# Kernel optimization log

Hardware: AMD Instinct MI355X
Metric: run time of the kernel (lower is better)

Reference implementation:

```python
import jax, jax.numpy as jnp
import numpy as np

WIN = 3
KER = 2 * WIN + 1
EPS = 1e-6


def _box_filter(x):
    """Separable 3D uniform box filter, mathematically identical to
    conv3d with a (1,1,k,k,k) kernel of ones/k^3 and padding=win.
    x: (B, 1, D, H, W) -> same shape."""
    dn = jax.lax.conv_dimension_numbers(x.shape, (1, 1, KER, 1, 1),
                                        ('NCDHW', 'OIDHW', 'NCDHW'))
    k1 = jnp.full((1, 1, KER, 1, 1), 1.0 / KER, dtype=x.dtype)
    k2 = jnp.full((1, 1, 1, KER, 1), 1.0 / KER, dtype=x.dtype)
    k3 = jnp.full((1, 1, 1, 1, KER), 1.0 / KER, dtype=x.dtype)
    x = jax.lax.conv_general_dilated(x, k1, (1, 1, 1),
                                     [(WIN, WIN), (0, 0), (0, 0)], dimension_numbers=dn)
    x = jax.lax.conv_general_dilated(x, k2, (1, 1, 1),
                                     [(0, 0), (WIN, WIN), (0, 0)], dimension_numbers=dn)
    x = jax.lax.conv_general_dilated(x, k3, (1, 1, 1),
                                     [(0, 0), (0, 0), (WIN, WIN)], dimension_numbers=dn)
    return x


def setup_inputs() -> dict:
    key = jax.random.key(0)
    kI, kJ = jax.random.split(key)
    shape = (2, 1, 160, 160, 160)
    I = jax.random.uniform(kI, shape, dtype=jnp.float32)
    J = jax.random.uniform(kJ, shape, dtype=jnp.float32)
    return {"I": I, "J": J}


def reference(I, J):
    I_mean = _box_filter(I)
    J_mean = _box_filter(J)
    I2_mean = _box_filter(I * I)
    J2_mean = _box_filter(J * J)
    IJ_mean = _box_filter(I * J)
    cross = IJ_mean - I_mean * J_mean
    I_var = I2_mean - I_mean * I_mean
    J_var = J2_mean - J_mean * J_mean
    lncc = cross * cross / (I_var * J_var + EPS)
    return -jnp.mean(lncc)
```

## Files before the change

### kernel.cpp

```cpp
#include <hip/hip_runtime.h>

#define DIM 160
#define TW 32
#define TH 16
#define RROWS (TH + 6)
#define CHUNK 16
#define NCHUNK (DIM / CHUNK)
#define NBATCH 2
#define NTOT 8192000.0f

__global__ __launch_bounds__(256) void lncc_fused_kernel(
    const float* __restrict__ I,
    const float* __restrict__ J,
    float* __restrict__ out)
{
    __shared__ __align__(16) float rs[2][5][RROWS][TW];
    __shared__ float wsum[4];

    const int tid = threadIdx.x;
    const int tx = tid & 15;
    const int ty = tid >> 4;
    const int rr = tid >> 3;
    const int rg = tid & 7;
    const bool rowActive = (rr < RROWS);

    const int tw0 = blockIdx.x * TW;
    const int th0 = blockIdx.y * TH;
    const int bz  = blockIdx.z;
    const int b     = bz / NCHUNK;
    const int chunk = bz - b * NCHUNK;
    const int z0  = chunk * CHUNK;

    const size_t plane = (size_t)DIM * DIM;
    const float* Ib = I + (size_t)b * DIM * plane;
    const float* Jb = J + (size_t)b * DIM * plane;

    const int gh = th0 + rr - 3;
    const bool rowValid = rowActive && ((unsigned)gh < (unsigned)DIM);
    const int gw0 = tw0 + 4 * rg - 4;
    const bool ok0 = (unsigned)gw0       <= (unsigned)(DIM - 4);
    const bool ok1 = (unsigned)(gw0 + 4) <= (unsigned)(DIM - 4);
    const bool ok2 = (unsigned)(gw0 + 8) <= (unsigned)(DIM - 4);
    const size_t rowbase = (size_t)gh * DIM + gw0;

    float rng[5][2][7];
#pragma unroll
    for (int f = 0; f < 5; ++f)
#pragma unroll
        for (int j = 0; j < 2; ++j)
#pragma unroll
            for (int k = 0; k < 7; ++k) rng[f][j][k] = 0.f;

    float S[5][2];
#pragma unroll
    for (int f = 0; f < 5; ++f) { S[f][0] = 0.f; S[f][1] = 0.f; }

    float acc = 0.f;
    int p = 0;

    for (int zin = z0 - 3; zin < z0 + CHUNK + 3; ++zin) {
        const bool zv = (zin >= 0) && (zin < DIM);
        float Cx[5], Cy[5];
#pragma unroll
        for (int f = 0; f < 5; ++f) { Cx[f] = 0.f; Cy[f] = 0.f; }

        if (zv) {
            if (rowActive) {
                float4 a0 = {0,0,0,0}, a1 = {0,0,0,0}, a2 = {0,0,0,0};
                float4 b0 = {0,0,0,0}, b1 = {0,0,0,0}, b2 = {0,0,0,0};
                if (rowValid) {
                    const float* Ip = Ib + (size_t)zin * plane + rowbase;
                    const float* Jp = Jb + (size_t)zin * plane + rowbase;
                    if (ok0) { a0 = *(const float4*)(Ip);     b0 = *(const float4*)(Jp);     }
                    if (ok1) { a1 = *(const float4*)(Ip + 4); b1 = *(const float4*)(Jp + 4); }
                    if (ok2) { a2 = *(const float4*)(Ip + 8); b2 = *(const float4*)(Jp + 8); }
                }
                float vI[12] = {a0.x,a0.y,a0.z,a0.w, a1.x,a1.y,a1.z,a1.w, a2.x,a2.y,a2.z,a2.w};
                float vJ[12] = {b0.x,b0.y,b0.z,b0.w, b1.x,b1.y,b1.z,b1.w, b2.x,b2.y,b2.z,b2.w};

                float sI=0.f, sJ=0.f, sI2=0.f, sJ2=0.f, sIJ=0.f;
#pragma unroll
                for (int i = 1; i < 8; ++i) {
                    float a = vI[i], c = vJ[i];
                    sI += a; sJ += c;
                    sI2 = fmaf(a, a, sI2);
                    sJ2 = fmaf(c, c, sJ2);
                    sIJ = fmaf(a, c, sIJ);
                }
                float wI[4], wJ[4], wI2[4], wJ2[4], wIJ[4];
                wI[0]=sI; wJ[0]=sJ; wI2[0]=sI2; wJ2[0]=sJ2; wIJ[0]=sIJ;
#pragma unroll
                for (int k = 1; k < 4; ++k) {
                    float an = vI[7+k], cn = vJ[7+k];
                    float ao = vI[k],   co = vJ[k];
                    sI  += an - ao;
                    sJ  += cn - co;
                    sI2 += fmaf(an, an, -(ao*ao));
                    sJ2 += fmaf(cn, cn, -(co*co));
                    sIJ += fmaf(an, cn, -(ao*co));
                    wI[k]=sI; wJ[k]=sJ; wI2[k]=sI2; wJ2[k]=sJ2; wIJ[k]=sIJ;
                }
                const int cc = 4 * rg;
                *(float4*)&rs[p][0][rr][cc] = make_float4(wI[0],  wI[1],  wI[2],  wI[3]);
                *(float4*)&rs[p][1][rr][cc] = make_float4(wJ[0],  wJ[1],  wJ[2],  wJ[3]);
                *(float4*)&rs[p][2][rr][cc] = make_float4(wI2[0], wI2[1], wI2[2], wI2[3]);
                *(float4*)&rs[p][3][rr][cc] = make_float4(wJ2[0], wJ2[1], wJ2[2], wJ2[3]);
                *(float4*)&rs[p][4][rr][cc] = make_float4(wIJ[0], wIJ[1], wIJ[2], wIJ[3]);
            }
            __syncthreads();

#pragma unroll
            for (int dr = 0; dr < 7; ++dr) {
                const int r = ty + dr;
#pragma unroll
                for (int f = 0; f < 5; ++f) {
                    const float2 v = *(const float2*)&rs[p][f][r][2 * tx];
                    Cx[f] += v.x;
                    Cy[f] += v.y;
                }
            }
            p ^= 1;
        }

#pragma unroll
        for (int f = 0; f < 5; ++f) {
            S[f][0] += Cx[f] - rng[f][0][0];
            S[f][1] += Cy[f] - rng[f][1][0];
#pragma unroll
            for (int k = 0; k < 6; ++k) {
                rng[f][0][k] = rng[f][0][k+1];
                rng[f][1][k] = rng[f][1][k+1];
            }
            rng[f][0][6] = Cx[f];
            rng[f][1][6] = Cy[f];
        }

        if (zin - 3 >= z0) {
            const float inv = 1.0f / 343.0f;
#pragma unroll
            for (int j = 0; j < 2; ++j) {
                float mI  = S[0][j] * inv;
                float mJ  = S[1][j] * inv;
                float mI2 = S[2][j] * inv;
                float mJ2 = S[3][j] * inv;
                float mIJ = S[4][j] * inv;
                float cross = mIJ - mI * mJ;
                float vI_ = mI2 - mI * mI;
                float vJ_ = mJ2 - mJ * mJ;
                acc += cross * cross / (vI_ * vJ_ + 1e-6f);
            }
        }
    }

#pragma unroll
    for (int off = 32; off > 0; off >>= 1)
        acc += __shfl_down(acc, off, 64);
    if ((tid & 63) == 0) wsum[tid >> 6] = acc;
    __syncthreads();
    if (tid == 0) {
        float t = wsum[0] + wsum[1] + wsum[2] + wsum[3];
        atomicAdd(out, t * (-1.0f / NTOT));
    }
}

extern "C" void kernel_launch(void* const* d_in, const int* in_sizes, int n_in,
                              void* d_out, int out_size, void* d_ws, size_t ws_size,
                              hipStream_t stream) {
    const float* I = (const float*)d_in[0];
    const float* J = (const float*)d_in[1];
    float* out = (float*)d_out;

    hipMemsetAsync(out, 0, sizeof(float), stream);

    dim3 grid(DIM / TW, DIM / TH, NBATCH * NCHUNK);
    dim3 block(256);
    lncc_fused_kernel<<<grid, block, 0, stream>>>(I, J, out);
}
```

Baseline: 153.5 us.

## Shrink z-chunks, unroll the ring buffer, and rescale the LNCC term to avoid division

Reduces the z-chunk from 16 to 10 slices, giving 16 chunks per batch and more blocks to spread across the CUs. The cost is more redundant halo slices per block: 16 loaded slices per 10 outputs instead of 22 per 16. The z ring buffer is now indexed by a compile-time slot in a 7-way unrolled step macro, replacing the per-step register shifting. The LNCC term works on raw sums scaled by 343, with a rescaled epsilon and a hardware reciprocal instead of a division. That adds a small approximation error from the fast reciprocal.

```diff
diff --git a/kernel.cpp b/kernel.cpp
--- a/kernel.cpp
+++ b/kernel.cpp
@@ -4,10 +4,65 @@
 #define TW 32
 #define TH 16
 #define RROWS (TH + 6)
-#define CHUNK 16
+#define CHUNK 10
 #define NCHUNK (DIM / CHUNK)
 #define NBATCH 2
 #define NTOT 8192000.0f
+#define EPS_S 13841.287f
+
+__device__ __forceinline__ void row_stage(
+    const float* __restrict__ Ip, const float* __restrict__ Jp,
+    bool rowValid, bool ok0, bool ok1, bool ok2,
+    float (* __restrict__ rsp)[RROWS][TW], int rr, int cc)
+{
+    float4 a0={0,0,0,0}, a1={0,0,0,0}, a2={0,0,0,0};
+    float4 b0={0,0,0,0}, b1={0,0,0,0}, b2={0,0,0,0};
+    if (rowValid) {
+        if (ok0) { a0 = *(const float4*)(Ip);     b0 = *(const float4*)(Jp);     }
+        if (ok1) { a1 = *(const float4*)(Ip + 4); b1 = *(const float4*)(Jp + 4); }
+        if (ok2) { a2 = *(const float4*)(Ip + 8); b2 = *(const float4*)(Jp + 8); }
+    }
+    float vI[12] = {a0.x,a0.y,a0.z,a0.w, a1.x,a1.y,a1.z,a1.w, a2.x,a2.y,a2.z,a2.w};
+    float vJ[12] = {b0.x,b0.y,b0.z,b0.w, b1.x,b1.y,b1.z,b1.w, b2.x,b2.y,b2.z,b2.w};
+
+    float sI=0.f, sJ=0.f, sI2=0.f, sJ2=0.f, sIJ=0.f;
+#pragma unroll
+    for (int i = 1; i < 8; ++i) {
+        float a = vI[i], c = vJ[i];
+        sI += a; sJ += c;
+        sI2 = fmaf(a, a, sI2);
+        sJ2 = fmaf(c, c, sJ2);
+        sIJ = fmaf(a, c, sIJ);
+    }
+    float wI[4], wJ[4], wI2[4], wJ2[4], wIJ[4];
+    wI[0]=sI; wJ[0]=sJ; wI2[0]=sI2; wJ2[0]=sJ2; wIJ[0]=sIJ;
+#pragma unroll
+    for (int k = 1; k < 4; ++k) {
+        float an = vI[7+k], cn = vJ[7+k];
+        float ao = vI[k],   co = vJ[k];
+        sI  += an - ao;
+        sJ  += cn - co;
+        sI2 += fmaf(an, an, -(ao*ao));
+        sJ2 += fmaf(cn, cn, -(co*co));
+        sIJ += fmaf(an, cn, -(ao*co));
+        wI[k]=sI; wJ[k]=sJ; wI2[k]=sI2; wJ2[k]=sJ2; wIJ[k]=sIJ;
+    }
+    *(float4*)&rsp[0][rr][cc] = make_float4(wI[0],  wI[1],  wI[2],  wI[3]);
+    *(float4*)&rsp[1][rr][cc] = make_float4(wJ[0],  wJ[1],  wJ[2],  wJ[3]);
+    *(float4*)&rsp[2][rr][cc] = make_float4(wI2[0], wI2[1], wI2[2], wI2[3]);
+    *(float4*)&rsp[3][rr][cc] = make_float4(wJ2[0], wJ2[1], wJ2[2], wJ2[3]);
+    *(float4*)&rsp[4][rr][cc] = make_float4(wIJ[0], wIJ[1], wIJ[2], wIJ[3]);
+}
+
+__device__ __forceinline__ float lncc_term(float SI, float SJ, float SI2,
+                                           float SJ2, float SIJ)
+{
+    float cross = fmaf(SIJ, 343.f, -(SI * SJ));
+    float vI    = fmaf(SI2, 343.f, -(SI * SI));
+    float vJ    = fmaf(SJ2, 343.f, -(SJ * SJ));
+    float den   = fmaf(vI, vJ, EPS_S);
+    return cross * cross * __builtin_amdgcn_rcpf(den);
+}
 
 __global__ __launch_bounds__(256) void lncc_fused_kernel(
     const float* __restrict__ I,
@@ -22,13 +77,14 @@
     const int ty = tid >> 4;
     const int rr = tid >> 3;
     const int rg = tid & 7;
+    const int cc = 4 * rg;
     const bool rowActive = (rr < RROWS);
 
     const int tw0 = blockIdx.x * TW;
     const int th0 = blockIdx.y * TH;
     const int bz  = blockIdx.z;
-    const int b     = bz / NCHUNK;
-    const int chunk = bz - b * NCHUNK;
+    const int b     = bz >> 4;
+    const int chunk = bz & 15;
     const int z0  = chunk * CHUNK;
 
     const size_t plane = (size_t)DIM * DIM;
@@ -37,120 +93,67 @@
 
     const int gh = th0 + rr - 3;
     const bool rowValid = rowActive && ((unsigned)gh < (unsigned)DIM);
-    const int gw0 = tw0 + 4 * rg - 4;
+    const int gw0 = tw0 + cc - 4;
     const bool ok0 = (unsigned)gw0       <= (unsigned)(DIM - 4);
     const bool ok1 = (unsigned)(gw0 + 4) <= (unsigned)(DIM - 4);
     const bool ok2 = (unsigned)(gw0 + 8) <= (unsigned)(DIM - 4);
-    const size_t rowbase = (size_t)gh * DIM + gw0;
+    const ptrdiff_t rowbase = (ptrdiff_t)gh * DIM + gw0;
+    const float* IpBase = Ib + rowbase;
+    const float* JpBase = Jb + rowbase;
 
-    float rng[5][2][7];
+    float rngx[5][7], rngy[5][7];
+    float Sx[5], Sy[5];
 #pragma unroll
-    for (int f = 0; f < 5; ++f)
+    for (int f = 0; f < 5; ++f) {
+        Sx[f] = 0.f; Sy[f] = 0.f;
 #pragma unroll
-        for (int j = 0; j < 2; ++j)
-#pragma unroll
-            for (int k = 0; k < 7; ++k) rng[f][j][k] = 0.f;
-
-    float S[5][2];
-#pragma unroll
-    for (int f = 0; f < 5; ++f) { S[f][0] = 0.f; S[f][1] = 0.f; }
+        for (int k = 0; k < 7; ++k) { rngx[f][k] = 0.f; rngy[f][k] = 0.f; }
+    }
 
     float acc = 0.f;
     int p = 0;
+    int zin = z0 - 3;
+    int s = 0;
 
-    for (int zin = z0 - 3; zin < z0 + CHUNK + 3; ++zin) {
-        const bool zv = (zin >= 0) && (zin < DIM);
-        float Cx[5], Cy[5];
-#pragma unroll
-        for (int f = 0; f < 5; ++f) { Cx[f] = 0.f; Cy[f] = 0.f; }
+#define STEP(SLOT) {                                                          \
+    const bool zv = ((unsigned)zin < (unsigned)DIM);                          \
+    float Cx[5] = {0.f,0.f,0.f,0.f,0.f};                                      \
+    float Cy[5] = {0.f,0.f,0.f,0.f,0.f};                                      \
+    if (zv) {                                                                 \
+        if (rowActive) {                                                      \
+            const float* Ip = IpBase + (ptrdiff_t)zin * (ptrdiff_t)plane;     \
+            const float* Jp = JpBase + (ptrdiff_t)zin * (ptrdiff_t)plane;     \
+            row_stage(Ip, Jp, rowValid, ok0, ok1, ok2, rs[p], rr, cc);        \
+        }                                                                     \
+        __syncthreads();                                                      \
+        _Pragma("unroll")                                                     \
+        for (int dr = 0; dr < 7; ++dr) {                                      \
+            _Pragma("unroll")                                                 \
+            for (int f = 0; f < 5; ++f) {                                     \
+                const float2 v = *(const float2*)&rs[p][f][ty + dr][2 * tx];  \
+                Cx[f] += v.x; Cy[f] += v.y;                                   \
+            }                                                                 \
+        }                                                                     \
+        p ^= 1;                                                               \
+    }                                                                         \
+    _Pragma("unroll")                                                         \
+    for (int f = 0; f < 5; ++f) {                                             \
+        Sx[f] += Cx[f] - rngx[f][SLOT]; rngx[f][SLOT] = Cx[f];                \
+        Sy[f] += Cy[f] - rngy[f][SLOT]; rngy[f][SLOT] = Cy[f];                \
+    }                                                                         \
+    if (s >= 6) {                                                             \
+        acc += lncc_term(Sx[0], Sx[1], Sx[2], Sx[3], Sx[4]);                  \
+        acc += lncc_term(Sy[0], Sy[1], Sy[2], Sy[3], Sy[4]);                  \
+    }                                                                         \
+    ++zin; ++s;                                                               \
+}
 
-        if (zv) {
-            if (rowActive) {
-                float4 a0 = {0,0,0,0}, a1 = {0,0,0,0}, a2 = {0,0,0,0};
-                float4 b0 = {0,0,0,0}, b1 = {0,0,0,0}, b2 = {0,0,0,0};
-                if (rowValid) {
-                    const float* Ip = Ib + (size_t)zin * plane + rowbase;
-                    const float* Jp = Jb + (size_t)zin * plane + rowbase;
-                    if (ok0) { a0 = *(const float4*)(Ip);     b0 = *(const float4*)(Jp);     }
-                    if (ok1) { a1 = *(const float4*)(Ip + 4); b1 = *(const float4*)(Jp + 4); }
-                    if (ok2) { a2 = *(const float4*)(Ip + 8); b2 = *(const float4*)(Jp + 8); }
-                }
-                float vI[12] = {a0.x,a0.y,a0.z,a0.w, a1.x,a1.y,a1.z,a1.w, a2.x,a2.y,a2.z,a2.w};
-                float vJ[12] = {b0.x,b0.y,b0.z,b0.w, b1.x,b1.y,b1.z,b1.w, b2.x,b2.y,b2.z,b2.w};
-
-                float sI=0.f, sJ=0.f, sI2=0.f, sJ2=0.f, sIJ=0.f;
-#pragma unroll
-                for (int i = 1; i < 8; ++i) {
-                    float a = vI[i], c = vJ[i];
-                    sI += a; sJ += c;
-                    sI2 = fmaf(a, a, sI2);
-                    sJ2 = fmaf(c, c, sJ2);
-                    sIJ = fmaf(a, c, sIJ);
-                }
-                float wI[4], wJ[4], wI2[4], wJ2[4], wIJ[4];
-                wI[0]=sI; wJ[0]=sJ; wI2[0]=sI2; wJ2[0]=sJ2; wIJ[0]=sIJ;
-#pragma unroll
-                for (int k = 1; k < 4; ++k) {
-                    float an = vI[7+k], cn = vJ[7+k];
-                    float ao = vI[k],   co = vJ[k];
-                    sI  += an - ao;
-                    sJ  += cn - co;
-                    sI2 += fmaf(an, an, -(ao*ao));
-                    sJ2 += fmaf(cn, cn, -(co*co));
-                    sIJ += fmaf(an, cn, -(ao*co));
-                    wI[k]=sI; wJ[k]=sJ; wI2[k]=sI2; wJ2[k]=sJ2; wIJ[k]=sIJ;
-                }
-                const int cc = 4 * rg;
-                *(float4*)&rs[p][0][rr][cc] = make_float4(wI[0],  wI[1],  wI[2],  wI[3]);
-                *(float4*)&rs[p][1][rr][cc] = make_float4(wJ[0],  wJ[1],  wJ[2],  wJ[3]);
-                *(float4*)&rs[p][2][rr][cc] = make_float4(wI2[0], wI2[1], wI2[2], wI2[3]);
-                *(float4*)&rs[p][3][rr][cc] = make_float4(wJ2[0], wJ2[1], wJ2[2], wJ2[3]);
-                *(float4*)&rs[p][4][rr][cc] = make_float4(wIJ[0], wIJ[1], wIJ[2], wIJ[3]);
-            }
-            __syncthreads();
-
-#pragma unroll
-            for (int dr = 0; dr < 7; ++dr) {
-                const int r = ty + dr;
-#pragma unroll
-                for (int f = 0; f < 5; ++f) {
-                    const float2 v = *(const float2*)&rs[p][f][r][2 * tx];
-                    Cx[f] += v.x;
-                    Cy[f] += v.y;
-                }
-            }
-            p ^= 1;
-        }
-
-#pragma unroll
-        for (int f = 0; f < 5; ++f) {
-            S[f][0] += Cx[f] - rng[f][0][0];
-            S[f][1] += Cy[f] - rng[f][1][0];
-#pragma unroll
-            for (int k = 0; k < 6; ++k) {
-                rng[f][0][k] = rng[f][0][k+1];
-                rng[f][1][k] = rng[f][1][k+1];
-            }
-            rng[f][0][6] = Cx[f];
-            rng[f][1][6] = Cy[f];
-        }
-
-        if (zin - 3 >= z0) {
-            const float inv = 1.0f / 343.0f;
-#pragma unroll
-            for (int j = 0; j < 2; ++j) {
-                float mI  = S[0][j] * inv;
-                float mJ  = S[1][j] * inv;
-                float mI2 = S[2][j] * inv;
-                float mJ2 = S[3][j] * inv;
-                float mIJ = S[4][j] * inv;
-                float cross = mIJ - mI * mJ;
-                float vI_ = mI2 - mI * mI;
-                float vJ_ = mJ2 - mJ * mJ;
-                acc += cross * cross / (vI_ * vJ_ + 1e-6f);
-            }
-        }
+#pragma unroll 1
+    for (int g = 0; g < 2; ++g) {
+        STEP(0) STEP(1) STEP(2) STEP(3) STEP(4) STEP(5) STEP(6)
     }
+    STEP(0) STEP(1)
+#undef STEP
 
 #pragma unroll
     for (int off = 32; off > 0; off >>= 1)
```

Result: slower. 167.0 us (+8.8%).
